# Performance work log

Hardware: AMD Instinct MI355X
Metric: run time of the kernel (lower is better)

The kernel has to match this reference:

```python
import math
import jax, jax.numpy as jnp
import numpy as np

N_HEADS = 16
D_EMBED = 1024
D_HEAD = D_EMBED // N_HEADS
B, S = 4, 2048


def setup_inputs() -> dict:
    key = jax.random.key(0)
    k1, k2, k3, k4, k5 = jax.random.split(key, 5)
    scale_in = 1.0 / math.sqrt(D_EMBED)
    return {
        "x": jax.random.normal(k1, (B, S, D_EMBED), dtype=jnp.float32),
        "w_in": jax.random.normal(k2, (3 * D_EMBED, D_EMBED), dtype=jnp.float32) * scale_in,
        "b_in": jax.random.normal(k3, (3 * D_EMBED,), dtype=jnp.float32) * 0.02,
        "w_out": jax.random.normal(k4, (D_EMBED, D_EMBED), dtype=jnp.float32) * scale_in,
        "b_out": jax.random.normal(k5, (D_EMBED,), dtype=jnp.float32) * 0.02,
        "causal_mask": 1,
    }


def reference(x, w_in, b_in, w_out, b_out, causal_mask):
    Bn, Sn, D = x.shape
    # fused QKV projection (torch Linear: x @ W.T + b)
    qkv = x @ w_in.T + b_in                       # (B, S, 3D)
    q, k, v = jnp.split(qkv, 3, axis=-1)
    def to_heads(t):
        return t.reshape(Bn, Sn, N_HEADS, D_HEAD).transpose(0, 2, 1, 3)  # (B,H,S,dh)
    q, k, v = to_heads(q), to_heads(k), to_heads(v)
    # manual scaled dot-product attention, full (B,H,S,S) scores
    scores = jnp.einsum("bhqd,bhkd->bhqk", q, k)
    if causal_mask:
        tri = jnp.triu(jnp.ones((Sn, Sn), dtype=bool), k=1)
        scores = jnp.where(tri, -jnp.inf, scores)
    scores = scores / math.sqrt(D_HEAD)
    weights = jax.nn.softmax(scores, axis=-1)
    out = jnp.einsum("bhqk,bhkd->bhqd", weights, v)  # (B,H,S,dh)
    out = out.transpose(0, 2, 1, 3).reshape(Bn, Sn, D)
    return out @ w_out.T + b_out
```

## Files before the change

kernel.cpp:

```cpp
#include <hip/hip_runtime.h>

typedef __bf16 bf16x8 __attribute__((ext_vector_type(8)));
typedef float  f32x4  __attribute__((ext_vector_type(4)));
typedef unsigned int uint;

__device__ inline unsigned short f2bf(float f) {
  union { float f; unsigned int u; } v; v.f = f;
  unsigned int u = v.u;
  unsigned int r = u + 0x7FFF + ((u >> 16) & 1);
  return (unsigned short)(r >> 16);
}

__device__ inline uint pack_bf16_rhu(float a, float b) {
  uint ua = __builtin_bit_cast(uint, a) + 0x8000u;
  uint ub = __builtin_bit_cast(uint, b) + 0x8000u;
  return __builtin_amdgcn_perm(ub, ua, 0x07060302u);
}

__device__ inline void load_lds16(const unsigned short* g, unsigned short* l) {
  __builtin_amdgcn_global_load_lds(
      (const __attribute__((address_space(1))) uint*)(g),
      (__attribute__((address_space(3))) uint*)(l), 16, 0, 0);
}

__device__ inline void cvt4(const float* in, unsigned short* out) {
  float4 f = *reinterpret_cast<const float4*>(in);
  ushort4 o;
  o.x = f2bf(f.x); o.y = f2bf(f.y); o.z = f2bf(f.z); o.w = f2bf(f.w);
  *reinterpret_cast<ushort4*>(out) = o;
}

__global__ void cvt_all(const float* __restrict__ x, const float* __restrict__ w_in,
                        const float* __restrict__ w_out,
                        unsigned short* __restrict__ x_bf,
                        unsigned short* __restrict__ w_in_bf,
                        unsigned short* __restrict__ w_out_bf) {
  const int n1 = 8192 * 1024, n2 = 3072 * 1024;
  int i = (blockIdx.x * blockDim.x + threadIdx.x) * 4;
  if (i < n1)            cvt4(x + i, x_bf + i);
  else if (i < n1 + n2)  cvt4(w_in + (i - n1), w_in_bf + (i - n1));
  else                   cvt4(w_out + (i - n1 - n2), w_out_bf + (i - n1 - n2));
}

template<bool OUT_BF16, bool VSPLIT>
__global__ __launch_bounds__(256) void gemm_bt128(
    const unsigned short* __restrict__ A,
    const unsigned short* __restrict__ B,
    const float* __restrict__ bias,
    void* __restrict__ Cout,
    unsigned short* __restrict__ vt,
    int M, int N, int K, int ldc, float scale, int ncut)
{
  __shared__ __attribute__((aligned(16))) unsigned short As[128 * 64];
  __shared__ __attribute__((aligned(16))) unsigned short Bs[128 * 64];

  const int t    = threadIdx.x;
  const int wave = t >> 6, lane = t & 63;
  const int l16  = lane & 15, quad = lane >> 4;
  const int wr = wave >> 1, wc = wave & 1;
  const int m0 = blockIdx.y * 128, n0 = blockIdx.x * 128;
  const int l8 = l16 & 7;

  f32x4 acc[4][4] = {};

  for (int k0 = 0; k0 < K; k0 += 64) {
#pragma unroll
    for (int i = 0; i < 4; ++i) {
      int chunk = i * 256 + t;
      int row = chunk >> 3, cb = chunk & 7;
      int gcb = cb ^ (row & 7);
      load_lds16(A + (size_t)(m0 + row) * K + k0 + gcb * 8, As + chunk * 8);
    }
#pragma unroll
    for (int i = 0; i < 4; ++i) {
      int chunk = i * 256 + t;
      int row = chunk >> 3, cb = chunk & 7;
      int gcb = cb ^ (row & 7);
      load_lds16(B + (size_t)(n0 + row) * K + k0 + gcb * 8, Bs + chunk * 8);
    }
    __syncthreads();
#pragma unroll
    for (int ks = 0; ks < 2; ++ks) {
      bf16x8 af[4], bfr[4];
#pragma unroll
      for (int mt = 0; mt < 4; ++mt)
        af[mt] = *(const bf16x8*)(As + (wr * 64 + mt * 16 + l16) * 64 +
                                  (((ks * 4 + quad) ^ l8) << 3));
#pragma unroll
      for (int nt = 0; nt < 4; ++nt)
        bfr[nt] = *(const bf16x8*)(Bs + (wc * 64 + nt * 16 + l16) * 64 +
                                   (((ks * 4 + quad) ^ l8) << 3));
#pragma unroll
      for (int mt = 0; mt < 4; ++mt)
#pragma unroll
        for (int nt = 0; nt < 4; ++nt)
          acc[mt][nt] = __builtin_amdgcn_mfma_f32_16x16x32_bf16(af[mt], bfr[nt], acc[mt][nt], 0, 0, 0);
    }
    __syncthreads();
  }

#pragma unroll
  for (int nt = 0; nt < 4; ++nt) {
    int col = n0 + wc * 64 + nt * 16 + l16;
    float bv = bias[col];
    float mlt = (col < ncut) ? scale : 1.0f;
#pragma unroll
    for (int mt = 0; mt < 4; ++mt) {
      int row0 = m0 + wr * 64 + mt * 16 + quad * 4;
      float v0 = (acc[mt][nt][0] + bv) * mlt;
      float v1 = (acc[mt][nt][1] + bv) * mlt;
      float v2 = (acc[mt][nt][2] + bv) * mlt;
      float v3 = (acc[mt][nt][3] + bv) * mlt;
      if (VSPLIT && col >= 2048) {
        int d = col - 2048, h = d >> 6, dd = d & 63;
        int bb = row0 >> 11, s = row0 & 2047;
        uint2 w;
        w.x = pack_bf16_rhu(v0, v1);
        w.y = pack_bf16_rhu(v2, v3);
        *(uint2*)(vt + ((size_t)((bb * 16 + h) * 64 + dd) * 2048 + s)) = w;
      } else {
#pragma unroll
        for (int r = 0; r < 4; ++r) {
          float v = (r == 0) ? v0 : (r == 1) ? v1 : (r == 2) ? v2 : v3;
          if (OUT_BF16)
            ((unsigned short*)Cout)[(size_t)(row0 + r) * ldc + col] = f2bf(v);
          else
            ((float*)Cout)[(size_t)(row0 + r) * ldc + col] = v;
        }
      }
    }
  }
}

__global__ __launch_bounds__(512) void attn(
    const unsigned short* __restrict__ qkv2,
    const unsigned short* __restrict__ vt,
    unsigned short* __restrict__ y,
    const int* __restrict__ flag)
{
  __shared__ __attribute__((aligned(16))) unsigned short Qs[128 * 64];
  __shared__ __attribute__((aligned(16))) unsigned short Ks[2][64 * 64];
  __shared__ __attribute__((aligned(16))) unsigned short Vs[2][64 * 64];

  const int t    = threadIdx.x;
  const int wave = t >> 6, lane = t & 63;
  const int l16  = lane & 15, quad = lane >> 4;
  const int l8   = l16 & 7;
  const int idx  = blockIdx.x;
  const int bh   = idx & 63;
  const int pair = idx >> 6;
  const int b = bh >> 4, h = bh & 15;
  const int causal = flag[0];

  const unsigned short* Qg  = qkv2 + (size_t)b * 2048 * 2048 + h * 64;
  const unsigned short* Kg  = Qg + 1024;
  const unsigned short* Vtg = vt + (size_t)bh * 64 * 2048;

  const int sr = t >> 2, sg = (t & 3) * 2;
  const int slot0 = sr * 64 + (((sg    ) ^ (sr & 7)) << 3);
  const int slot1 = sr * 64 + (((sg + 1) ^ (sr & 7)) << 3);
  const int kr = t >> 3, kg = t & 7;
  const int kslot = kr * 64 + ((kg ^ (kr & 7)) << 3);

  unsigned short* Ps = Qs;

  for (int half = 0; half < 2; ++half) {
    const int qt = half ? pair : (15 - pair);
    const int q0 = qt * 128;
    const int jmax = causal ? 2 * qt + 1 : 31;

    const unsigned short* kptr = Kg + (size_t)kr * 2048 + kg * 8;
    const unsigned short* vptr = Vtg + (size_t)kr * 2048 + kg * 8;
    uint4 kreg = *(const uint4*)kptr;
    uint4 vreg = *(const uint4*)vptr;
    {
      const unsigned short* src = Qg + (size_t)(q0 + sr) * 2048 + sg * 8;
      *(uint4*)(Qs + slot0) = *(const uint4*)src;
      *(uint4*)(Qs + slot1) = *(const uint4*)(src + 8);
    }
    __syncthreads();
    bf16x8 qf[2];
    qf[0] = *(const bf16x8*)(Qs + (wave * 16 + l16) * 64 + (((0 + quad) ^ l8) << 3));
    qf[1] = *(const bf16x8*)(Qs + (wave * 16 + l16) * 64 + (((4 + quad) ^ l8) << 3));
    __syncthreads();

    *(uint4*)(Ks[0] + kslot) = kreg;
    *(uint4*)(Vs[0] + kslot) = vreg;
    kptr += 64 * 2048;
    vptr += 64;
    if (jmax > 0) {
      kreg = *(const uint4*)kptr;
      vreg = *(const uint4*)vptr;
    }
    __syncthreads();

    f32x4 ot[4] = {};
    float l_lane = 0.f;
    const int q_glob = q0 + wave * 16 + l16;
    const int wq_max = q0 + wave * 16 + 15;

    for (int j = 0; j <= jmax; ++j) {
      const int cur = j & 1;
      if (j < jmax) {
        *(uint4*)(Ks[cur ^ 1] + kslot) = kreg;
        *(uint4*)(Vs[cur ^ 1] + kslot) = vreg;
        if (j + 1 < jmax) {
          kptr += 64 * 2048;
          vptr += 64;
          kreg = *(const uint4*)kptr;
          vreg = *(const uint4*)vptr;
        }
      }

      const bool active = !causal || ((j << 6) <= wq_max);
      if (active) {
        f32x4 st[4] = {};
        __builtin_amdgcn_s_setprio(1);
#pragma unroll
        for (int ks = 0; ks < 2; ++ks) {
#pragma unroll
          for (int mt = 0; mt < 4; ++mt) {
            bf16x8 kf = *(const bf16x8*)(Ks[cur] + (mt * 16 + l16) * 64 +
                                         (((ks * 4 + quad) ^ l8) << 3));
            st[mt] = __builtin_amdgcn_mfma_f32_16x16x32_bf16(kf, qf[ks], st[mt], 0, 0, 0);
          }
        }
        __builtin_amdgcn_s_setprio(0);

        const int kv0 = j << 6;
        const bool diag = (causal != 0) && (kv0 + 63 > q_glob);
#pragma unroll
        for (int mt = 0; mt < 4; ++mt) {
          float p[4];
#pragma unroll
          for (int r = 0; r < 4; ++r) {
            float pv = __builtin_amdgcn_exp2f(st[mt][r]);
            if (diag) {
              int kv = kv0 + mt * 16 + quad * 4 + r;
              if (kv > q_glob) pv = 0.f;
            }
            p[r] = pv;
          }
          l_lane += (p[0] + p[1]) + (p[2] + p[3]);
          uint2 w;
          w.x = pack_bf16_rhu(p[0], p[1]);
          w.y = pack_bf16_rhu(p[2], p[3]);
          *(uint2*)(Ps + (wave * 16 + l16) * 64 +
                    ((((mt * 2 + (quad >> 1)) ^ l8) << 3) + (quad & 1) * 4)) = w;
        }
        __threadfence_block();

        __builtin_amdgcn_s_setprio(1);
#pragma unroll
        for (int ks = 0; ks < 2; ++ks) {
          bf16x8 pf = *(const bf16x8*)(Ps + (wave * 16 + l16) * 64 +
                                       (((ks * 4 + quad) ^ l8) << 3));
#pragma unroll
          for (int mt = 0; mt < 4; ++mt) {
            bf16x8 vf = *(const bf16x8*)(Vs[cur] + (mt * 16 + l16) * 64 +
                                         (((ks * 4 + quad) ^ l8) << 3));
            ot[mt] = __builtin_amdgcn_mfma_f32_16x16x32_bf16(vf, pf, ot[mt], 0, 0, 0);
          }
        }
        __builtin_amdgcn_s_setprio(0);
      }
      __syncthreads();
    }

    l_lane += __shfl_xor(l_lane, 16);
    l_lane += __shfl_xor(l_lane, 32);
    float inv = 1.f / l_lane;

#pragma unroll
    for (int mt = 0; mt < 4; ++mt) {
      uint2 w;
      w.x = pack_bf16_rhu(ot[mt][0] * inv, ot[mt][1] * inv);
      w.y = pack_bf16_rhu(ot[mt][2] * inv, ot[mt][3] * inv);
      *(uint2*)(Ps + (wave * 16 + l16) * 64 +
                ((((mt * 2 + (quad >> 1)) ^ l8) << 3) + (quad & 1) * 4)) = w;
    }
    __syncthreads();
    {
      size_t base = ((size_t)b * 2048 + q0 + sr) * 1024 + h * 64 + sg * 8;
      *(uint4*)(y + base)     = *(const uint4*)(Ps + slot0);
      *(uint4*)(y + base + 8) = *(const uint4*)(Ps + slot1);
    }
    __syncthreads();
  }
}

extern "C" void kernel_launch(void* const* d_in, const int* in_sizes, int n_in,
                              void* d_out, int out_size, void* d_ws, size_t ws_size,
                              hipStream_t stream) {
  const float* x     = (const float*)d_in[0];
  const float* w_in  = (const float*)d_in[1];
  const float* b_in  = (const float*)d_in[2];
  const float* w_out = (const float*)d_in[3];
  const float* b_out = (const float*)d_in[4];
  const int*   cmask = (const int*)d_in[5];

  char* ws = (char*)d_ws;
  unsigned short* x_bf     = (unsigned short*)(ws);
  unsigned short* w_in_bf  = (unsigned short*)(ws + 16777216);
  unsigned short* w_out_bf = (unsigned short*)(ws + 23068672);
  unsigned short* qkv2_bf  = (unsigned short*)(ws + 25165824);
  unsigned short* vt_bf    = (unsigned short*)(ws + 58720256);
  unsigned short* y_bf     = (unsigned short*)(ws + 75497472);

  const int ntot = (8192 + 3072 + 1024) * 1024;
  cvt_all<<<dim3(ntot / 4 / 256), 256, 0, stream>>>(x, w_in, w_out, x_bf, w_in_bf, w_out_bf);

  gemm_bt128<true, true><<<dim3(24, 64), 256, 0, stream>>>(
      x_bf, w_in_bf, b_in, qkv2_bf, vt_bf, 8192, 3072, 1024, 2048,
      0.18033688011112042f, 1024);

  attn<<<dim3(512), 512, 0, stream>>>(qkv2_bf, vt_bf, y_bf, cmask);

  gemm_bt128<false, false><<<dim3(8, 64), 256, 0, stream>>>(
      y_bf, w_out_bf, b_out, d_out, nullptr, 8192, 1024, 1024, 1024, 1.0f, 0);
}
```

Before: 241.8 us.

## Shrink attention query tile to 64 rows with 4 waves and double the grid

The attention kernel moves from 128-row query tiles with 8 waves to 64-row tiles with 4 waves and launches twice as many blocks. Tiles are still paired so causal work balances within each block. K/V staging is remapped so 256 threads each load two 16-byte chunks, and the per-wave active check is dropped because every wave in a 64-row tile covers the same key range. The aim is better occupancy and finer load balance; the cost is that each K/V tile loaded into LDS is now reused by half as many query rows.

```diff
diff --git a/kernel.cpp b/kernel.cpp
--- a/kernel.cpp
+++ b/kernel.cpp
@@ -132,13 +132,13 @@
   }
 }
 
-__global__ __launch_bounds__(512) void attn(
+__global__ __launch_bounds__(256) void attn(
     const unsigned short* __restrict__ qkv2,
     const unsigned short* __restrict__ vt,
     unsigned short* __restrict__ y,
     const int* __restrict__ flag)
 {
-  __shared__ __attribute__((aligned(16))) unsigned short Qs[128 * 64];
+  __shared__ __attribute__((aligned(16))) unsigned short Qs[64 * 64];
   __shared__ __attribute__((aligned(16))) unsigned short Ks[2][64 * 64];
   __shared__ __attribute__((aligned(16))) unsigned short Vs[2][64 * 64];
 
@@ -148,7 +148,7 @@
   const int l8   = l16 & 7;
   const int idx  = blockIdx.x;
   const int bh   = idx & 63;
-  const int pair = idx >> 6;
+  const int kp   = idx >> 6;
   const int b = bh >> 4, h = bh & 15;
   const int causal = flag[0];
 
@@ -159,20 +159,23 @@
   const int sr = t >> 2, sg = (t & 3) * 2;
   const int slot0 = sr * 64 + (((sg    ) ^ (sr & 7)) << 3);
   const int slot1 = sr * 64 + (((sg + 1) ^ (sr & 7)) << 3);
-  const int kr = t >> 3, kg = t & 7;
-  const int kslot = kr * 64 + ((kg ^ (kr & 7)) << 3);
+  const int vb = t & 3;
+  const int vslot0 = sr * 64 + ((( vb    ) ^ (sr & 7)) << 3);
+  const int vslot1 = sr * 64 + (((vb + 4) ^ (sr & 7)) << 3);
+  const unsigned short* vrow = Vtg + (size_t)sr * 2048;
+  const unsigned short* krow = Kg + (size_t)sr * 2048 + sg * 8;
 
   unsigned short* Ps = Qs;
 
   for (int half = 0; half < 2; ++half) {
-    const int qt = half ? pair : (15 - pair);
-    const int q0 = qt * 128;
-    const int jmax = causal ? 2 * qt + 1 : 31;
-
-    const unsigned short* kptr = Kg + (size_t)kr * 2048 + kg * 8;
-    const unsigned short* vptr = Vtg + (size_t)kr * 2048 + kg * 8;
-    uint4 kreg = *(const uint4*)kptr;
-    uint4 vreg = *(const uint4*)vptr;
+    const int qt = half ? kp : (31 - kp);
+    const int q0 = qt * 64;
+    const int jmax = causal ? qt : 31;
+
+    uint4 kreg0 = *(const uint4*)krow;
+    uint4 kreg1 = *(const uint4*)(krow + 8);
+    uint4 vreg0 = *(const uint4*)(vrow + vb * 8);
+    uint4 vreg1 = *(const uint4*)(vrow + vb * 8 + 32);
     {
       const unsigned short* src = Qg + (size_t)(q0 + sr) * 2048 + sg * 8;
       *(uint4*)(Qs + slot0) = *(const uint4*)src;
@@ -184,86 +187,87 @@
     qf[1] = *(const bf16x8*)(Qs + (wave * 16 + l16) * 64 + (((4 + quad) ^ l8) << 3));
     __syncthreads();
 
-    *(uint4*)(Ks[0] + kslot) = kreg;
-    *(uint4*)(Vs[0] + kslot) = vreg;
-    kptr += 64 * 2048;
-    vptr += 64;
+    *(uint4*)(Ks[0] + slot0)  = kreg0;
+    *(uint4*)(Ks[0] + slot1)  = kreg1;
+    *(uint4*)(Vs[0] + vslot0) = vreg0;
+    *(uint4*)(Vs[0] + vslot1) = vreg1;
     if (jmax > 0) {
-      kreg = *(const uint4*)kptr;
-      vreg = *(const uint4*)vptr;
+      kreg0 = *(const uint4*)(krow + (size_t)64 * 2048);
+      kreg1 = *(const uint4*)(krow + (size_t)64 * 2048 + 8);
+      vreg0 = *(const uint4*)(vrow + 64 + vb * 8);
+      vreg1 = *(const uint4*)(vrow + 64 + vb * 8 + 32);
     }
     __syncthreads();
 
     f32x4 ot[4] = {};
     float l_lane = 0.f;
     const int q_glob = q0 + wave * 16 + l16;
-    const int wq_max = q0 + wave * 16 + 15;
 
     for (int j = 0; j <= jmax; ++j) {
       const int cur = j & 1;
       if (j < jmax) {
-        *(uint4*)(Ks[cur ^ 1] + kslot) = kreg;
-        *(uint4*)(Vs[cur ^ 1] + kslot) = vreg;
+        *(uint4*)(Ks[cur ^ 1] + slot0)  = kreg0;
+        *(uint4*)(Ks[cur ^ 1] + slot1)  = kreg1;
+        *(uint4*)(Vs[cur ^ 1] + vslot0) = vreg0;
+        *(uint4*)(Vs[cur ^ 1] + vslot1) = vreg1;
         if (j + 1 < jmax) {
-          kptr += 64 * 2048;
-          vptr += 64;
-          kreg = *(const uint4*)kptr;
-          vreg = *(const uint4*)vptr;
-        }
-      }
-
-      const bool active = !causal || ((j << 6) <= wq_max);
-      if (active) {
-        f32x4 st[4] = {};
-        __builtin_amdgcn_s_setprio(1);
-#pragma unroll
-        for (int ks = 0; ks < 2; ++ks) {
-#pragma unroll
-          for (int mt = 0; mt < 4; ++mt) {
-            bf16x8 kf = *(const bf16x8*)(Ks[cur] + (mt * 16 + l16) * 64 +
-                                         (((ks * 4 + quad) ^ l8) << 3));
-            st[mt] = __builtin_amdgcn_mfma_f32_16x16x32_bf16(kf, qf[ks], st[mt], 0, 0, 0);
+          const int kvn = (j + 2) * 64;
+          kreg0 = *(const uint4*)(krow + (size_t)kvn * 2048);
+          kreg1 = *(const uint4*)(krow + (size_t)kvn * 2048 + 8);
+          vreg0 = *(const uint4*)(vrow + kvn + vb * 8);
+          vreg1 = *(const uint4*)(vrow + kvn + vb * 8 + 32);
+        }
+      }
+
+      f32x4 st[4] = {};
+      __builtin_amdgcn_s_setprio(1);
+#pragma unroll
+      for (int ks = 0; ks < 2; ++ks) {
+#pragma unroll
+        for (int mt = 0; mt < 4; ++mt) {
+          bf16x8 kf = *(const bf16x8*)(Ks[cur] + (mt * 16 + l16) * 64 +
+                                       (((ks * 4 + quad) ^ l8) << 3));
+          st[mt] = __builtin_amdgcn_mfma_f32_16x16x32_bf16(kf, qf[ks], st[mt], 0, 0, 0);
+        }
+      }
+      __builtin_amdgcn_s_setprio(0);
+
+      const bool diag = (causal != 0) && (j == qt);
+      const int kv0 = j << 6;
+#pragma unroll
+      for (int mt = 0; mt < 4; ++mt) {
+        float p[4];
+#pragma unroll
+        for (int r = 0; r < 4; ++r) {
+          float pv = __builtin_amdgcn_exp2f(st[mt][r]);
+          if (diag) {
+            int kv = kv0 + mt * 16 + quad * 4 + r;
+            if (kv > q_glob) pv = 0.f;
           }
-        }
-        __builtin_amdgcn_s_setprio(0);
-
-        const int kv0 = j << 6;
-        const bool diag = (causal != 0) && (kv0 + 63 > q_glob);
+          p[r] = pv;
+        }
+        l_lane += (p[0] + p[1]) + (p[2] + p[3]);
+        uint2 w;
+        w.x = pack_bf16_rhu(p[0], p[1]);
+        w.y = pack_bf16_rhu(p[2], p[3]);
+        *(uint2*)(Ps + (wave * 16 + l16) * 64 +
+                  ((((mt * 2 + (quad >> 1)) ^ l8) << 3) + (quad & 1) * 4)) = w;
+      }
+      __threadfence_block();
+
+      __builtin_amdgcn_s_setprio(1);
+#pragma unroll
+      for (int ks = 0; ks < 2; ++ks) {
+        bf16x8 pf = *(const bf16x8*)(Ps + (wave * 16 + l16) * 64 +
+                                     (((ks * 4 + quad) ^ l8) << 3));
 #pragma unroll
         for (int mt = 0; mt < 4; ++mt) {
-          float p[4];
-#pragma unroll
-          for (int r = 0; r < 4; ++r) {
-            float pv = __builtin_amdgcn_exp2f(st[mt][r]);
-            if (diag) {
-              int kv = kv0 + mt * 16 + quad * 4 + r;
-              if (kv > q_glob) pv = 0.f;
-            }
-            p[r] = pv;
-          }
-          l_lane += (p[0] + p[1]) + (p[2] + p[3]);
-          uint2 w;
-          w.x = pack_bf16_rhu(p[0], p[1]);
-          w.y = pack_bf16_rhu(p[2], p[3]);
-          *(uint2*)(Ps + (wave * 16 + l16) * 64 +
-                    ((((mt * 2 + (quad >> 1)) ^ l8) << 3) + (quad & 1) * 4)) = w;
-        }
-        __threadfence_block();
-
-        __builtin_amdgcn_s_setprio(1);
-#pragma unroll
-        for (int ks = 0; ks < 2; ++ks) {
-          bf16x8 pf = *(const bf16x8*)(Ps + (wave * 16 + l16) * 64 +
+          bf16x8 vf = *(const bf16x8*)(Vs[cur] + (mt * 16 + l16) * 64 +
                                        (((ks * 4 + quad) ^ l8) << 3));
-#pragma unroll
-          for (int mt = 0; mt < 4; ++mt) {
-            bf16x8 vf = *(const bf16x8*)(Vs[cur] + (mt * 16 + l16) * 64 +
-                                         (((ks * 4 + quad) ^ l8) << 3));
-            ot[mt] = __builtin_amdgcn_mfma_f32_16x16x32_bf16(vf, pf, ot[mt], 0, 0, 0);
-          }
-        }
-        __builtin_amdgcn_s_setprio(0);
-      }
+          ot[mt] = __builtin_amdgcn_mfma_f32_16x16x32_bf16(vf, pf, ot[mt], 0, 0, 0);
+        }
+      }
+      __builtin_amdgcn_s_setprio(0);
       __syncthreads();
     }
 
@@ -314,7 +318,7 @@
       x_bf, w_in_bf, b_in, qkv2_bf, vt_bf, 8192, 3072, 1024, 2048,
       0.18033688011112042f, 1024);
 
-  attn<<<dim3(512), 512, 0, stream>>>(qkv2_bf, vt_bf, y_bf, cmask);
+  attn<<<dim3(1024), 256, 0, stream>>>(qkv2_bf, vt_bf, y_bf, cmask);
 
   gemm_bt128<false, false><<<dim3(8, 64), 256, 0, stream>>>(
       y_bf, w_out_bf, b_out, d_out, nullptr, 8192, 1024, 1024, 1024, 1.0f, 0);
```

Result: slower. 252.5 us (+4.4%).
